# Kernel tuning notes

Measured on AMD Instinct MI355X. Metric: run time of the kernel, lower is better.

## Reference

```python
import jax, jax.numpy as jnp
import numpy as np
from jax import lax

DN = ('NCH', 'OIH', 'NCH')

def _conv(x, w, b, pad):
    # x: [B, C, L]; replication (edge) pad then VALID conv, per nn.ReplicationPad1d + Conv1d
    if pad != (0, 0):
        x = jnp.pad(x, ((0, 0), (0, 0), pad), mode='edge')
    y = lax.conv_general_dilated(x, w, (1,), 'VALID', dimension_numbers=DN)
    return y + b[None, :, None]

def setup_inputs() -> dict:
    key = jax.random.key(0)
    ks = jax.random.split(key, 11)
    B, L, C, H = 32, 512, 300, 512
    s = 1.0 / np.sqrt(C)
    inp = {
        'x': jax.random.normal(ks[0], (B, L, C), jnp.float32),
        'w1': jax.random.normal(ks[1], (C, C, 1), jnp.float32) * s,
        'b1': jax.random.normal(ks[2], (C,), jnp.float32) * s,
        'w2': jax.random.normal(ks[3], (C, C, 2), jnp.float32) * s,
        'b2': jax.random.normal(ks[4], (C,), jnp.float32) * s,
        'w3': jax.random.normal(ks[5], (C, C, 3), jnp.float32) * s,
        'b3': jax.random.normal(ks[6], (C,), jnp.float32) * s,
        'w7': jax.random.normal(ks[7], (C, C, 7), jnp.float32) * s,
        'b7': jax.random.normal(ks[8], (C,), jnp.float32) * s,
        'slp_w': jax.random.normal(ks[9], (H, 5 * C), jnp.float32) * (1.0 / np.sqrt(5 * C)),
        'slp_b': jax.random.normal(ks[10], (H,), jnp.float32) * (1.0 / np.sqrt(5 * C)),
    }
    return inp

def reference(x, w1, b1, w2, b2, w3, b3, w7, b7, slp_w, slp_b):
    xc = jnp.transpose(x, (0, 2, 1))  # [B, C, L]
    x1 = jnp.tanh(_conv(xc, w1, b1, (0, 0)))
    x2 = jnp.tanh(_conv(xc, w2, b2, (0, 1)))
    x3 = jnp.tanh(_conv(xc, w3, b3, (1, 1)))
    x5 = x3  # faithful to the original bug: x5 = self.conv3(x)
    x7 = jnp.tanh(_conv(xc, w7, b7, (3, 3)))
    # concat channels -> [B, L, 1500], then linear + tanh -> [B, L, 512]
    h = jnp.concatenate([x1, x2, x3, x5, x7], axis=1)  # [B, 5C, L]
    h = jnp.transpose(h, (0, 2, 1))  # [B, L, 5C]
    out = jnp.tanh(jnp.einsum('blc,hc->blh', h, slp_w) + slp_b)
    return out
```

## Files before the change

### kernel.cpp

```cpp
#include <hip/hip_runtime.h>
#include <hip/hip_bf16.h>

typedef __attribute__((ext_vector_type(8))) short short8;
typedef __attribute__((ext_vector_type(16))) float floatx16;

#define Bn 32
#define Ln 512
#define Cn 300
#define Hn 512
#define Nn (Bn*Ln)
#define XBP 518
#define XBC 320
#define HK 1216
#define LDSTC 72

#define XROWS 134
#define XSZ (XROWS*LDSTC)
#define HSROWS 128
#define HSSZ (HSROWS*LDSTC)

#define XB_ELEMS (Bn*XBP*XBC)
#define WB_ELEMS 1597440
#define WC_ELEMS (Hn*HK)
#define XB_OFF 0
#define WB_OFF (XB_OFF + XB_ELEMS)
#define WC_OFF (WB_OFF + WB_ELEMS)
#define HB_OFF (WC_OFF + WC_ELEMS)

__device__ __forceinline__ float fast_tanh(float x) {
    float ax = __builtin_fabsf(x);
    float t  = __expf(-2.f * ax);
    float r  = __builtin_fmaf(-2.f * t, __frcp_rn(1.f + t), 1.f);
    return __builtin_copysignf(r, x);
}

__global__ void prep_all(const float* __restrict__ x,
                         const float* __restrict__ w1, const float* __restrict__ w2,
                         const float* __restrict__ w3, const float* __restrict__ w7,
                         const float* __restrict__ slp_w,
                         __hip_bfloat16* __restrict__ wsb) {
    int idx = blockIdx.x * 256 + threadIdx.x;
    if (idx < XB_ELEMS) {
        int c = idx % XBC;
        int t = idx / XBC;
        int p = t % XBP;
        int b = t / XBP;
        int l = p - 3;
        l = l < 0 ? 0 : (l > Ln - 1 ? Ln - 1 : l);
        float v = (c < Cn) ? x[(b * Ln + l) * Cn + c] : 0.f;
        wsb[idx] = __float2bfloat16(v);
    } else if (idx < WB_OFF + WB_ELEMS) {
        int r = idx - WB_OFF, taps; const float* w;
        if (r < 122880)       { taps = 1; w = w1; }
        else if (r < 368640)  { taps = 2; w = w2; r -= 122880; }
        else if (r < 737280)  { taps = 3; w = w3; r -= 368640; }
        else                  { taps = 7; w = w7; r -= 737280; }
        int e    = r & 7;
        int lane = (r >> 3) & 63;
        int f    = (r >> 9) & 15;
        int rt   = r >> 13;
        int t    = rt % taps;
        int mc   = rt / taps;
        int ch   = mc % 5;
        int mt   = mc / 5;
        int ks = f >> 2, mq = f & 3;
        int m = mt * 128 + mq * 32 + (lane & 31);
        int c = ch * 64 + ks * 16 + (lane >> 5) * 8 + e;
        float v = (m < Cn && c < Cn) ? w[(m * Cn + c) * taps + t] : 0.f;
        wsb[idx] = __float2bfloat16(v);
    } else if (idx < WC_OFF + WC_ELEMS) {
        int r = idx - WC_OFF;
        int e    = r & 7;
        int lane = (r >> 3) & 63;
        int f    = (r >> 9) & 15;
        int mc   = r >> 13;
        int ch   = mc % 19;
        int mt4  = mc / 19;
        int ks = f >> 2, mq = f & 3;
        int h = mt4 * 128 + mq * 32 + (lane & 31);
        int k = ch * 64 + ks * 16 + (lane >> 5) * 8 + e;
        const float* row = slp_w + h * 1500;
        float v;
        if (k < 600)       v = row[k];
        else if (k < 900)  v = row[k] + row[k + 300];
        else if (k < 1200) v = row[k + 300];
        else               v = 0.f;
        wsb[idx] = __float2bfloat16(v);
    }
}

#define MFMA __builtin_amdgcn_mfma_f32_32x32x16_bf16

template<int TAPS, int LEAD>
__device__ __forceinline__ void conv_body(
        const short* __restrict__ xbs, const short* __restrict__ wsp,
        const float* __restrict__ bias, int cid, int mt, int nt,
        __hip_bfloat16* __restrict__ hbuf, short* xs) {
    const int tid  = threadIdx.x;
    const int lane = tid & 63;
    const int wave = tid >> 6;
    const int wn = wave & 1, wm = wave >> 1;
    const int lr = lane & 31;
    const int lk = (lane >> 5) << 3;
    const int TRIG = (TAPS >= 3) ? TAPS - 2 : 0;

    floatx16 acc[2][2];
#pragma unroll
    for (int i = 0; i < 2; i++)
#pragma unroll
        for (int j = 0; j < 2; j++)
#pragma unroll
            for (int r = 0; r < 16; r++) acc[i][j][r] = 0.f;

    short8 bA[8], bB[8], st[5];

#pragma unroll
    for (int i = 0; i < 5; ++i) {
        int j = tid + 256 * i;
        if (i < 4 || j < 1072)
            st[i] = *(const short8*)&xbs[(j >> 3) * XBC + ((j & 7) << 3)];
    }
#pragma unroll
    for (int ks = 0; ks < 4; ++ks)
#pragma unroll
        for (int mf = 0; mf < 2; ++mf)
            bA[ks * 2 + mf] = *(const short8*)&wsp[(ks * 4 + wm * 2 + mf) * 512 + lane * 8];
#pragma unroll
    for (int i = 0; i < 5; ++i) {
        int j = tid + 256 * i;
        if (i < 4 || j < 1072)
            *(short8*)&xs[(j >> 3) * LDSTC + ((j & 7) << 3)] = st[i];
    }
    __syncthreads();

    for (int c5 = 0; c5 < 5; ++c5) {
        const short* cur = xs + (c5 & 1) * XSZ;
        short* nxt = xs + ((c5 + 1) & 1) * XSZ;
        const int c0n = (c5 + 1) * 64;
#pragma unroll
        for (int t = 0; t < TAPS; ++t) {
            if (!(c5 == 4 && t == TAPS - 1)) {
                const short* wtn = (t + 1 < TAPS) ? wsp + (c5 * TAPS + t + 1) * 8192
                                                  : wsp + ((c5 + 1) * TAPS) * 8192;
#pragma unroll
                for (int ks = 0; ks < 4; ++ks)
#pragma unroll
                    for (int mf = 0; mf < 2; ++mf)
                        bB[ks * 2 + mf] = *(const short8*)&wtn[(ks * 4 + wm * 2 + mf) * 512 + lane * 8];
            }
            if (t == TRIG && c5 < 4) {
#pragma unroll
                for (int i = 0; i < 5; ++i) {
                    int j = tid + 256 * i;
                    if (i < 4 || j < 1072)
                        st[i] = *(const short8*)&xbs[(j >> 3) * XBC + c0n + ((j & 7) << 3)];
                }
            }
            const int sh = t - LEAD + 3;
            const int ar = (wn * 64 + lr + sh) * LDSTC + lk;
#pragma unroll
            for (int ks = 0; ks < 4; ++ks) {
                short8 a0 = *(const short8*)&cur[ar + ks * 16];
                short8 a1 = *(const short8*)&cur[ar + 32 * LDSTC + ks * 16];
                acc[0][0] = MFMA(a0, bA[ks * 2 + 0], acc[0][0], 0, 0, 0);
                acc[0][1] = MFMA(a0, bA[ks * 2 + 1], acc[0][1], 0, 0, 0);
                acc[1][0] = MFMA(a1, bA[ks * 2 + 0], acc[1][0], 0, 0, 0);
                acc[1][1] = MFMA(a1, bA[ks * 2 + 1], acc[1][1], 0, 0, 0);
            }
            if (!(c5 == 4 && t == TAPS - 1)) {
#pragma unroll
                for (int f = 0; f < 8; ++f) bA[f] = bB[f];
            }
        }
        if (c5 < 4) {
#pragma unroll
            for (int i = 0; i < 5; ++i) {
                int j = tid + 256 * i;
                if (i < 4 || j < 1072)
                    *(short8*)&nxt[(j >> 3) * LDSTC + ((j & 7) << 3)] = st[i];
            }
        }
        __syncthreads();
    }

#pragma unroll
    for (int mi = 0; mi < 2; ++mi) {
        int mloc = mt * 128 + wm * 64 + mi * 32 + lr;
        if (mloc < Cn) {
            float bv = bias[mloc];
            int col = cid * Cn + mloc;
#pragma unroll
            for (int ni = 0; ni < 2; ++ni) {
                floatx16 v = acc[ni][mi];
#pragma unroll
                for (int reg = 0; reg < 16; ++reg) {
                    int nl = wn * 64 + ni * 32 + (reg & 3) + ((reg >> 2) << 3) + ((lane >> 5) << 2);
                    int n = nt * 128 + nl;
                    hbuf[n * HK + col] = __float2bfloat16(fast_tanh(v[reg] + bv));
                }
            }
        }
    }
}

__global__ __launch_bounds__(256, 2) void conv_kernel(
        const __hip_bfloat16* __restrict__ xbg, const __hip_bfloat16* __restrict__ Wbg,
        const float* __restrict__ bias1, const float* __restrict__ bias2,
        const float* __restrict__ bias3, const float* __restrict__ bias7,
        __hip_bfloat16* __restrict__ hbuf) {
    __shared__ __align__(16) short xs[2 * XSZ];

    const int nt = blockIdx.x;
    const int my = blockIdx.y;
    const int g  = my / 3;
    const int mt = my % 3;

    const int b  = nt >> 2;
    const int l0 = (nt & 3) << 7;
    const short* xbs = (const short*)xbg + (b * XBP + l0) * XBC;
    const short* wb  = (const short*)Wbg;

    if (g == 0)      conv_body<7, 3>(xbs, wb + 737280 + mt * 7 * 40960, bias7, 3, mt, nt, hbuf, xs);
    else if (g == 1) conv_body<3, 1>(xbs, wb + 368640 + mt * 3 * 40960, bias3, 2, mt, nt, hbuf, xs);
    else if (g == 2) conv_body<2, 0>(xbs, wb + 122880 + mt * 2 * 40960, bias2, 1, mt, nt, hbuf, xs);
    else             conv_body<1, 0>(xbs, wb +      0 + mt * 1 * 40960, bias1, 0, mt, nt, hbuf, xs);
}

__global__ __launch_bounds__(256, 2) void linear_kernel(
        const __hip_bfloat16* __restrict__ hbufg, const __hip_bfloat16* __restrict__ Wcg,
        const float* __restrict__ slp_b, float* __restrict__ out) {
    __shared__ __align__(16) short hs[2 * HSSZ];

    const int tid  = threadIdx.x;
    const int lane = tid & 63;
    const int wave = tid >> 6;
    const int wn = wave & 1, wm = wave >> 1;
    const int lr = lane & 31;
    const int lk = (lane >> 5) << 3;

    const int nt  = blockIdx.x;
    const int mt4 = blockIdx.y;

    const short* hbp = (const short*)hbufg + nt * 128 * HK;
    const short* wcp = (const short*)Wcg + mt4 * 155648;

    const int srow = tid >> 1;
    const int scc  = (tid & 1) << 5;
    floatx16 acc[2][2];
#pragma unroll
    for (int i = 0; i < 2; i++)
#pragma unroll
        for (int j = 0; j < 2; j++)
#pragma unroll
            for (int r = 0; r < 16; r++) acc[i][j][r] = 0.f;

    short8 bA[8], bB[8], st[4];
    (void)srow; (void)scc;

#pragma unroll
    for (int i = 0; i < 4; ++i) {
        int j = tid + 256 * i;
        st[i] = *(const short8*)&hbp[(j >> 3) * HK + ((j & 7) << 3)];
    }
#pragma unroll
    for (int ks = 0; ks < 4; ++ks)
#pragma unroll
        for (int mf = 0; mf < 2; ++mf)
            bA[ks * 2 + mf] = *(const short8*)&wcp[(ks * 4 + wm * 2 + mf) * 512 + lane * 8];
#pragma unroll
    for (int i = 0; i < 4; ++i) {
        int j = tid + 256 * i;
        *(short8*)&hs[(j >> 3) * LDSTC + ((j & 7) << 3)] = st[i];
    }
    __syncthreads();

    for (int ch = 0; ch < 19; ++ch) {
        const short* cur = hs + (ch & 1) * HSSZ;
        short* nxt = hs + ((ch + 1) & 1) * HSSZ;
        if (ch < 18) {
            const short* wtn = wcp + (ch + 1) * 8192;
#pragma unroll
            for (int ks = 0; ks < 4; ++ks)
#pragma unroll
                for (int mf = 0; mf < 2; ++mf)
                    bB[ks * 2 + mf] = *(const short8*)&wtn[(ks * 4 + wm * 2 + mf) * 512 + lane * 8];
            const int c0n = (ch + 1) * 64;
#pragma unroll
            for (int i = 0; i < 4; ++i) {
                int j = tid + 256 * i;
                st[i] = *(const short8*)&hbp[(j >> 3) * HK + c0n + ((j & 7) << 3)];
            }
        }
        const int ar = (wn * 64 + lr) * LDSTC + lk;
#pragma unroll
        for (int ks = 0; ks < 4; ++ks) {
            short8 a0 = *(const short8*)&cur[ar + ks * 16];
            short8 a1 = *(const short8*)&cur[ar + 32 * LDSTC + ks * 16];
            acc[0][0] = MFMA(a0, bA[ks * 2 + 0], acc[0][0], 0, 0, 0);
            acc[0][1] = MFMA(a0, bA[ks * 2 + 1], acc[0][1], 0, 0, 0);
            acc[1][0] = MFMA(a1, bA[ks * 2 + 0], acc[1][0], 0, 0, 0);
            acc[1][1] = MFMA(a1, bA[ks * 2 + 1], acc[1][1], 0, 0, 0);
        }
        if (ch < 18) {
#pragma unroll
            for (int f = 0; f < 8; ++f) bA[f] = bB[f];
#pragma unroll
            for (int i = 0; i < 4; ++i) {
                int j = tid + 256 * i;
                *(short8*)&nxt[(j >> 3) * LDSTC + ((j & 7) << 3)] = st[i];
            }
        }
        __syncthreads();
    }

#pragma unroll
    for (int mi = 0; mi < 2; ++mi) {
        int h = mt4 * 128 + wm * 64 + mi * 32 + lr;
        float bv = slp_b[h];
#pragma unroll
        for (int ni = 0; ni < 2; ++ni) {
            floatx16 v = acc[ni][mi];
#pragma unroll
            for (int reg = 0; reg < 16; ++reg) {
                int nl = wn * 64 + ni * 32 + (reg & 3) + ((reg >> 2) << 3) + ((lane >> 5) << 2);
                int n = nt * 128 + nl;
                out[n * Hn + h] = fast_tanh(v[reg] + bv);
            }
        }
    }
}


extern "C" void kernel_launch(void* const* d_in, const int* in_sizes, int n_in,
                              void* d_out, int out_size, void* d_ws, size_t ws_size,
                              hipStream_t stream) {
    const float* x     = (const float*)d_in[0];
    const float* w1    = (const float*)d_in[1];
    const float* b1    = (const float*)d_in[2];
    const float* w2    = (const float*)d_in[3];
    const float* b2    = (const float*)d_in[4];
    const float* w3    = (const float*)d_in[5];
    const float* b3    = (const float*)d_in[6];
    const float* w7    = (const float*)d_in[7];
    const float* b7    = (const float*)d_in[8];
    const float* slp_w = (const float*)d_in[9];
    const float* slp_b = (const float*)d_in[10];

    __hip_bfloat16* wsb = (__hip_bfloat16*)d_ws;

    const int prep_total = XB_ELEMS + WB_ELEMS + WC_ELEMS;
    prep_all<<<(prep_total + 255) / 256, 256, 0, stream>>>(x, w1, w2, w3, w7, slp_w, wsb);

    conv_kernel<<<dim3(128, 12), 256, 0, stream>>>(wsb + XB_OFF, wsb + WB_OFF,
                                                   b1, b2, b3, b7, wsb + HB_OFF);
    linear_kernel<<<dim3(128, 4), 256, 0, stream>>>(wsb + HB_OFF, wsb + WC_OFF,
                                                    slp_b, (float*)d_out);
}
```

Baseline: 187.3 us.

## Write conv output in MFMA fragment layout and drop LDS staging in linear kernel

The conv epilogue now swaps the MFMA operand order so each lane holds four consecutive output channels. It writes packed bf16x4 values straight into a pre-swizzled fragment layout, with channel groups padded to 304, instead of scattered 2-byte stores. The linear kernel loads its hidden-state and weight fragments directly from global memory into double-buffered registers, with no shared memory or barriers, and writes float4 outputs. This trades LDS reuse across waves for more global/L2 traffic and higher register pressure, and the weight-packing index math changes to match the new K layout.

```diff
diff --git a/kernel.cpp b/kernel.cpp
--- a/kernel.cpp
+++ b/kernel.cpp
@@ -2,6 +2,7 @@
 #include <hip/hip_bf16.h>
 
 typedef __attribute__((ext_vector_type(8))) short short8;
+typedef __attribute__((ext_vector_type(4))) short short4v;
 typedef __attribute__((ext_vector_type(16))) float floatx16;
 
 #define Bn 32
@@ -16,8 +17,6 @@
 
 #define XROWS 134
 #define XSZ (XROWS*LDSTC)
-#define HSROWS 128
-#define HSSZ (HSROWS*LDSTC)
 
 #define XB_ELEMS (Bn*XBP*XBC)
 #define WB_ELEMS 1597440
@@ -79,12 +78,16 @@
         int ks = f >> 2, mq = f & 3;
         int h = mt4 * 128 + mq * 32 + (lane & 31);
         int k = ch * 64 + ks * 16 + (lane >> 5) * 8 + e;
+        int cid = k / 304;
+        int mk  = k - cid * 304;
         const float* row = slp_w + h * 1500;
-        float v;
-        if (k < 600)       v = row[k];
-        else if (k < 900)  v = row[k] + row[k + 300];
-        else if (k < 1200) v = row[k + 300];
-        else               v = 0.f;
+        float v = 0.f;
+        if (mk < 300) {
+            if (cid == 0)      v = row[mk];
+            else if (cid == 1) v = row[300 + mk];
+            else if (cid == 2) v = row[600 + mk] + row[900 + mk];
+            else               v = row[1200 + mk];
+        }
         wsb[idx] = __float2bfloat16(v);
     }
 }
@@ -95,7 +98,7 @@
 __device__ __forceinline__ void conv_body(
         const short* __restrict__ xbs, const short* __restrict__ wsp,
         const float* __restrict__ bias, int cid, int mt, int nt,
-        __hip_bfloat16* __restrict__ hbuf, short* xs) {
+        short* __restrict__ hbuf, short* xs) {
     const int tid  = threadIdx.x;
     const int lane = tid & 63;
     const int wave = tid >> 6;
@@ -112,7 +115,7 @@
 #pragma unroll
             for (int r = 0; r < 16; r++) acc[i][j][r] = 0.f;
 
-    short8 bA[8], bB[8], st[5];
+    short8 wA[8], wB[8], st[5];
 
 #pragma unroll
     for (int i = 0; i < 5; ++i) {
@@ -124,7 +127,7 @@
     for (int ks = 0; ks < 4; ++ks)
 #pragma unroll
         for (int mf = 0; mf < 2; ++mf)
-            bA[ks * 2 + mf] = *(const short8*)&wsp[(ks * 4 + wm * 2 + mf) * 512 + lane * 8];
+            wA[ks * 2 + mf] = *(const short8*)&wsp[(ks * 4 + wm * 2 + mf) * 512 + lane * 8];
 #pragma unroll
     for (int i = 0; i < 5; ++i) {
         int j = tid + 256 * i;
@@ -146,7 +149,7 @@
                 for (int ks = 0; ks < 4; ++ks)
 #pragma unroll
                     for (int mf = 0; mf < 2; ++mf)
-                        bB[ks * 2 + mf] = *(const short8*)&wtn[(ks * 4 + wm * 2 + mf) * 512 + lane * 8];
+                        wB[ks * 2 + mf] = *(const short8*)&wtn[(ks * 4 + wm * 2 + mf) * 512 + lane * 8];
             }
             if (t == TRIG && c5 < 4) {
 #pragma unroll
@@ -157,19 +160,19 @@
                 }
             }
             const int sh = t - LEAD + 3;
-            const int ar = (wn * 64 + lr + sh) * LDSTC + lk;
+            const int br = (wn * 64 + lr + sh) * LDSTC + lk;
 #pragma unroll
             for (int ks = 0; ks < 4; ++ks) {
-                short8 a0 = *(const short8*)&cur[ar + ks * 16];
-                short8 a1 = *(const short8*)&cur[ar + 32 * LDSTC + ks * 16];
-                acc[0][0] = MFMA(a0, bA[ks * 2 + 0], acc[0][0], 0, 0, 0);
-                acc[0][1] = MFMA(a0, bA[ks * 2 + 1], acc[0][1], 0, 0, 0);
-                acc[1][0] = MFMA(a1, bA[ks * 2 + 0], acc[1][0], 0, 0, 0);
-                acc[1][1] = MFMA(a1, bA[ks * 2 + 1], acc[1][1], 0, 0, 0);
+                short8 x0 = *(const short8*)&cur[br + ks * 16];
+                short8 x1 = *(const short8*)&cur[br + 32 * LDSTC + ks * 16];
+                acc[0][0] = MFMA(wA[ks * 2 + 0], x0, acc[0][0], 0, 0, 0);
+                acc[0][1] = MFMA(wA[ks * 2 + 0], x1, acc[0][1], 0, 0, 0);
+                acc[1][0] = MFMA(wA[ks * 2 + 1], x0, acc[1][0], 0, 0, 0);
+                acc[1][1] = MFMA(wA[ks * 2 + 1], x1, acc[1][1], 0, 0, 0);
             }
             if (!(c5 == 4 && t == TAPS - 1)) {
 #pragma unroll
-                for (int f = 0; f < 8; ++f) bA[f] = bB[f];
+                for (int f = 0; f < 8; ++f) wA[f] = wB[f];
             }
         }
         if (c5 < 4) {
@@ -184,23 +187,27 @@
     }
 
 #pragma unroll
-    for (int mi = 0; mi < 2; ++mi) {
-        int mloc = mt * 128 + wm * 64 + mi * 32 + lr;
-        if (mloc < Cn) {
-            float bv = bias[mloc];
-            int col = cid * Cn + mloc;
-#pragma unroll
-            for (int ni = 0; ni < 2; ++ni) {
-                floatx16 v = acc[ni][mi];
-#pragma unroll
-                for (int reg = 0; reg < 16; ++reg) {
-                    int nl = wn * 64 + ni * 32 + (reg & 3) + ((reg >> 2) << 3) + ((lane >> 5) << 2);
-                    int n = nt * 128 + nl;
-                    hbuf[n * HK + col] = __float2bfloat16(fast_tanh(v[reg] + bv));
+    for (int mi = 0; mi < 2; ++mi)
+#pragma unroll
+        for (int ni = 0; ni < 2; ++ni) {
+            floatx16 v = acc[mi][ni];
+            const int n5 = nt * 4 + wn * 2 + ni;
+#pragma unroll
+            for (int q = 0; q < 4; ++q) {
+                int mb = mt * 128 + wm * 64 + mi * 32 + q * 8 + ((lane >> 5) << 2);
+                if (mb < Cn) {
+                    float4 bv = *(const float4*)&bias[mb];
+                    short4v pk;
+                    pk[0] = ((__hip_bfloat16_raw)__float2bfloat16(fast_tanh(v[q*4+0] + bv.x))).x;
+                    pk[1] = ((__hip_bfloat16_raw)__float2bfloat16(fast_tanh(v[q*4+1] + bv.y))).x;
+                    pk[2] = ((__hip_bfloat16_raw)__float2bfloat16(fast_tanh(v[q*4+2] + bv.z))).x;
+                    pk[3] = ((__hip_bfloat16_raw)__float2bfloat16(fast_tanh(v[q*4+3] + bv.w))).x;
+                    int k0  = cid * 304 + mb;
+                    int off = (n5 * 76 + (k0 >> 4)) * 512 + (lr + ((q & 1) << 5)) * 8 + ((lane >> 5) << 2);
+                    *(short4v*)&hbuf[off] = pk;
                 }
             }
         }
-    }
 }
 
 __global__ __launch_bounds__(256, 2) void conv_kernel(
@@ -219,33 +226,30 @@
     const int l0 = (nt & 3) << 7;
     const short* xbs = (const short*)xbg + (b * XBP + l0) * XBC;
     const short* wb  = (const short*)Wbg;
-
-    if (g == 0)      conv_body<7, 3>(xbs, wb + 737280 + mt * 7 * 40960, bias7, 3, mt, nt, hbuf, xs);
-    else if (g == 1) conv_body<3, 1>(xbs, wb + 368640 + mt * 3 * 40960, bias3, 2, mt, nt, hbuf, xs);
-    else if (g == 2) conv_body<2, 0>(xbs, wb + 122880 + mt * 2 * 40960, bias2, 1, mt, nt, hbuf, xs);
-    else             conv_body<1, 0>(xbs, wb +      0 + mt * 1 * 40960, bias1, 0, mt, nt, hbuf, xs);
+    short* hb = (short*)hbuf;
+
+    if (g == 0)      conv_body<7, 3>(xbs, wb + 737280 + mt * 7 * 40960, bias7, 3, mt, nt, hb, xs);
+    else if (g == 1) conv_body<3, 1>(xbs, wb + 368640 + mt * 3 * 40960, bias3, 2, mt, nt, hb, xs);
+    else if (g == 2) conv_body<2, 0>(xbs, wb + 122880 + mt * 2 * 40960, bias2, 1, mt, nt, hb, xs);
+    else             conv_body<1, 0>(xbs, wb +      0 + mt * 1 * 40960, bias1, 0, mt, nt, hb, xs);
 }
 
 __global__ __launch_bounds__(256, 2) void linear_kernel(
         const __hip_bfloat16* __restrict__ hbufg, const __hip_bfloat16* __restrict__ Wcg,
         const float* __restrict__ slp_b, float* __restrict__ out) {
-    __shared__ __align__(16) short hs[2 * HSSZ];
-
     const int tid  = threadIdx.x;
     const int lane = tid & 63;
     const int wave = tid >> 6;
-    const int wn = wave & 1, wm = wave >> 1;
-    const int lr = lane & 31;
-    const int lk = (lane >> 5) << 3;
-
-    const int nt  = blockIdx.x;
-    const int mt4 = blockIdx.y;
-
-    const short* hbp = (const short*)hbufg + nt * 128 * HK;
-    const short* wcp = (const short*)Wcg + mt4 * 155648;
-
-    const int srow = tid >> 1;
-    const int scc  = (tid & 1) << 5;
+    const int lr   = lane & 31;
+
+    const int nt64 = blockIdx.x;
+    const int hw   = blockIdx.y * 4 + wave;
+    const int mt4  = hw >> 1;
+    const int mq0  = (hw & 1) * 2;
+
+    const short* hb = (const short*)hbufg;
+    const short* wc = (const short*)Wcg;
+
     floatx16 acc[2][2];
 #pragma unroll
     for (int i = 0; i < 2; i++)
@@ -254,80 +258,57 @@
 #pragma unroll
             for (int r = 0; r < 16; r++) acc[i][j][r] = 0.f;
 
-    short8 bA[8], bB[8], st[4];
-    (void)srow; (void)scc;
-
-#pragma unroll
-    for (int i = 0; i < 4; ++i) {
-        int j = tid + 256 * i;
-        st[i] = *(const short8*)&hbp[(j >> 3) * HK + ((j & 7) << 3)];
-    }
-#pragma unroll
-    for (int ks = 0; ks < 4; ++ks)
-#pragma unroll
-        for (int mf = 0; mf < 2; ++mf)
-            bA[ks * 2 + mf] = *(const short8*)&wcp[(ks * 4 + wm * 2 + mf) * 512 + lane * 8];
-#pragma unroll
-    for (int i = 0; i < 4; ++i) {
-        int j = tid + 256 * i;
-        *(short8*)&hs[(j >> 3) * LDSTC + ((j & 7) << 3)] = st[i];
-    }
-    __syncthreads();
-
+    short8 wf[2][8], hf[2][8];
+
+#define LOAD_CHUNK(ch, p)                                                                 \
+    {                                                                                     \
+        _Pragma("unroll")                                                                 \
+        for (int ks = 0; ks < 4; ++ks)                                                    \
+            _Pragma("unroll")                                                             \
+            for (int ni = 0; ni < 2; ++ni)                                                \
+                hf[p][ks * 2 + ni] = *(const short8*)                                     \
+                    &hb[(((nt64 * 2 + ni) * 76) + (ch) * 4 + ks) * 512 + lane * 8];       \
+        _Pragma("unroll")                                                                 \
+        for (int ks = 0; ks < 4; ++ks)                                                    \
+            _Pragma("unroll")                                                             \
+            for (int mi = 0; mi < 2; ++mi)                                                \
+                wf[p][ks * 2 + mi] = *(const short8*)                                     \
+                    &wc[((mt4 * 19 + (ch)) * 16 + ks * 4 + mq0 + mi) * 512 + lane * 8];   \
+    }
+
+    LOAD_CHUNK(0, 0)
+#pragma unroll
     for (int ch = 0; ch < 19; ++ch) {
-        const short* cur = hs + (ch & 1) * HSSZ;
-        short* nxt = hs + ((ch + 1) & 1) * HSSZ;
-        if (ch < 18) {
-            const short* wtn = wcp + (ch + 1) * 8192;
-#pragma unroll
-            for (int ks = 0; ks < 4; ++ks)
-#pragma unroll
-                for (int mf = 0; mf < 2; ++mf)
-                    bB[ks * 2 + mf] = *(const short8*)&wtn[(ks * 4 + wm * 2 + mf) * 512 + lane * 8];
-            const int c0n = (ch + 1) * 64;
-#pragma unroll
-            for (int i = 0; i < 4; ++i) {
-                int j = tid + 256 * i;
-                st[i] = *(const short8*)&hbp[(j >> 3) * HK + c0n + ((j & 7) << 3)];
-            }
-        }
-        const int ar = (wn * 64 + lr) * LDSTC + lk;
+        const int p = ch & 1;
+        if (ch < 18) LOAD_CHUNK(ch + 1, p ^ 1)
 #pragma unroll
         for (int ks = 0; ks < 4; ++ks) {
-            short8 a0 = *(const short8*)&cur[ar + ks * 16];
-            short8 a1 = *(const short8*)&cur[ar + 32 * LDSTC + ks * 16];
-            acc[0][0] = MFMA(a0, bA[ks * 2 + 0], acc[0][0], 0, 0, 0);
-            acc[0][1] = MFMA(a0, bA[ks * 2 + 1], acc[0][1], 0, 0, 0);
-            acc[1][0] = MFMA(a1, bA[ks * 2 + 0], acc[1][0], 0, 0, 0);
-            acc[1][1] = MFMA(a1, bA[ks * 2 + 1], acc[1][1], 0, 0, 0);
-        }
-        if (ch < 18) {
-#pragma unroll
-            for (int f = 0; f < 8; ++f) bA[f] = bB[f];
-#pragma unroll
-            for (int i = 0; i < 4; ++i) {
-                int j = tid + 256 * i;
-                *(short8*)&nxt[(j >> 3) * LDSTC + ((j & 7) << 3)] = st[i];
-            }
-        }
-        __syncthreads();
-    }
-
-#pragma unroll
-    for (int mi = 0; mi < 2; ++mi) {
-        int h = mt4 * 128 + wm * 64 + mi * 32 + lr;
-        float bv = slp_b[h];
+            acc[0][0] = MFMA(wf[p][ks * 2 + 0], hf[p][ks * 2 + 0], acc[0][0], 0, 0, 0);
+            acc[0][1] = MFMA(wf[p][ks * 2 + 0], hf[p][ks * 2 + 1], acc[0][1], 0, 0, 0);
+            acc[1][0] = MFMA(wf[p][ks * 2 + 1], hf[p][ks * 2 + 0], acc[1][0], 0, 0, 0);
+            acc[1][1] = MFMA(wf[p][ks * 2 + 1], hf[p][ks * 2 + 1], acc[1][1], 0, 0, 0);
+        }
+    }
+#undef LOAD_CHUNK
+
+#pragma unroll
+    for (int mi = 0; mi < 2; ++mi)
 #pragma unroll
         for (int ni = 0; ni < 2; ++ni) {
-            floatx16 v = acc[ni][mi];
-#pragma unroll
-            for (int reg = 0; reg < 16; ++reg) {
-                int nl = wn * 64 + ni * 32 + (reg & 3) + ((reg >> 2) << 3) + ((lane >> 5) << 2);
-                int n = nt * 128 + nl;
-                out[n * Hn + h] = fast_tanh(v[reg] + bv);
-            }
-        }
-    }
+            floatx16 v = acc[mi][ni];
+            const int n = nt64 * 64 + ni * 32 + lr;
+#pragma unroll
+            for (int q = 0; q < 4; ++q) {
+                int h0 = hw * 64 + mi * 32 + q * 8 + ((lane >> 5) << 2);
+                float4 bv = *(const float4*)&slp_b[h0];
+                float4 o;
+                o.x = fast_tanh(v[q * 4 + 0] + bv.x);
+                o.y = fast_tanh(v[q * 4 + 1] + bv.y);
+                o.z = fast_tanh(v[q * 4 + 2] + bv.z);
+                o.w = fast_tanh(v[q * 4 + 3] + bv.w);
+                *(float4*)&out[n * Hn + h0] = o;
+            }
+        }
 }
 
 
@@ -353,6 +334,6 @@
 
     conv_kernel<<<dim3(128, 12), 256, 0, stream>>>(wsb + XB_OFF, wsb + WB_OFF,
                                                    b1, b2, b3, b7, wsb + HB_OFF);
-    linear_kernel<<<dim3(128, 4), 256, 0, stream>>>(wsb + HB_OFF, wsb + WC_OFF,
+    linear_kernel<<<dim3(256, 2), 256, 0, stream>>>(wsb + HB_OFF, wsb + WC_OFF,
                                                     slp_b, (float*)d_out);
 }
```

Measured after the change: 204.9 us. 9.4% more time.
